# Performance work log

Hardware: AMD Instinct MI355X
Metric: run time of the kernel (lower is better)

The kernel has to match this reference:

```python
import jax, jax.numpy as jnp
import numpy as np
import math

BS, QL, KL = 2, 2048, 2048
H, D = 16, 64          # n_heads, cell_dim
QS = KS = VS = 1024    # query/key/value feature sizes
HD = H * D


def setup_inputs() -> dict:
    key = jax.random.key(0)
    ks = jax.random.split(key, 12)
    s_in = 1.0 / math.sqrt(QS)
    s_hd = 1.0 / math.sqrt(HD)
    return {
        "query": jax.random.normal(ks[0], (BS, QL, QS), jnp.float32),
        "key": jax.random.normal(ks[1], (BS, KL, KS), jnp.float32),
        "value": jax.random.normal(ks[2], (BS, KL, VS), jnp.float32),
        # nn.Linear weights stored as [in, out] for x @ W + b
        "Wq_w": jax.random.normal(ks[3], (QS, HD), jnp.float32) * s_in,
        "Wq_b": jax.random.normal(ks[4], (HD,), jnp.float32) * s_in,
        "Wk_w": jax.random.normal(ks[5], (KS, HD), jnp.float32) * s_in,
        "Wk_b": jax.random.normal(ks[6], (HD,), jnp.float32) * s_in,
        "Wv_w": jax.random.normal(ks[7], (VS, HD), jnp.float32) * s_in,
        "Wv_b": jax.random.normal(ks[8], (HD,), jnp.float32) * s_in,
        "Wo_w": jax.random.normal(ks[9], (HD, HD), jnp.float32) * s_hd,
        "Wo_b": jax.random.normal(ks[10], (HD,), jnp.float32) * s_hd,
    }


def reference(query, key, value, Wq_w, Wq_b, Wk_w, Wk_b, Wv_w, Wv_b, Wo_w, Wo_b):
    bs, ql, _ = query.shape
    kl = key.shape[1]
    # project and split heads; torch .chunk along dim 2 == head-major reshape
    q = (query @ Wq_w + Wq_b).reshape(bs, ql, H, D).transpose(0, 2, 1, 3)  # bhqd
    k = (key @ Wk_w + Wk_b).reshape(bs, kl, H, D).transpose(0, 2, 1, 3)    # bhkd
    v = (value @ Wv_w + Wv_b).reshape(bs, kl, H, D).transpose(0, 2, 1, 3)  # bhkd
    scores = jnp.einsum("bhqd,bhkd->bhqk", q, k) / jnp.sqrt(jnp.float32(D))
    # log_softmax(...).exp() == softmax (use_mask=False path)
    w = jax.nn.softmax(scores, axis=-1)
    heads = jnp.einsum("bhqk,bhkd->bhqd", w, v)
    out = heads.transpose(0, 2, 1, 3).reshape(bs, ql, HD)  # concat heads on dim 2
    return out @ Wo_w + Wo_b
```

## Files before the change

### kernel.cpp

```cpp
#include <hip/hip_runtime.h>

#define BSZ 2
#define SEQ 2048
#define NH 16
#define DHD 64
#define HDIM 1024
#define FS 1024
#define MR (BSZ*SEQ)
#define L2E 1.4426950408889634f

typedef __bf16 bf16x8 __attribute__((ext_vector_type(8)));
typedef __bf16 bf16x2t __attribute__((ext_vector_type(2)));
typedef float f32x4 __attribute__((ext_vector_type(4)));
typedef float f32x16 __attribute__((ext_vector_type(16)));
typedef unsigned short u16;
typedef unsigned int u32;
typedef u32 u32x4 __attribute__((ext_vector_type(4)));

__device__ __forceinline__ u16 f2bf(float f) {
  u32 x = __float_as_uint(f);
  return (u16)((x + 0x7fffu + ((x >> 16) & 1u)) >> 16);
}

__device__ __forceinline__ u32 pack2bf(float a, float b) {
  bf16x2t t = {(__bf16)a, (__bf16)b};
  return __builtin_bit_cast(u32, t);
}

__device__ __forceinline__ void gload16(const void* g, void* l) {
  __builtin_amdgcn_global_load_lds(
      (const __attribute__((address_space(1))) u32*)g,
      (__attribute__((address_space(3))) u32*)l, 16, 0, 0);
}

__global__ __launch_bounds__(256) void cast3_k(const float* __restrict__ q,
                                               const float* __restrict__ k,
                                               const float* __restrict__ v,
                                               u16* __restrict__ dst, int n4) {
  int i = blockIdx.x * 256 + threadIdx.x;
  const int st = gridDim.x * 256;
  const int tot = 3 * n4;
  for (; i < tot; i += st) {
    const int arr = i >> 20;
    const int idx = i & (n4 - 1);
    const float* src = arr == 0 ? q : arr == 1 ? k : v;
    float4 vv = ((const float4*)src)[idx];
    ushort4 o;
    o.x = f2bf(vv.x); o.y = f2bf(vv.y); o.z = f2bf(vv.z); o.w = f2bf(vv.w);
    ((ushort4*)dst)[i] = o;
  }
}

__global__ __launch_bounds__(256) void transw4_k(
    const float* __restrict__ W0, const float* __restrict__ W1,
    const float* __restrict__ W2, const float* __restrict__ W3,
    u16* __restrict__ WTbase) {
  __shared__ float t[32][33];
  const int z = blockIdx.z;
  const float* W = z == 0 ? W0 : z == 1 ? W1 : z == 2 ? W2 : W3;
  u16* WT = WTbase + (size_t)z * FS * HDIM;
  const int tx = threadIdx.x, ty = threadIdx.y;
  const int c0 = blockIdx.x * 32, r0 = blockIdx.y * 32;
#pragma unroll
  for (int i = 0; i < 4; i++)
    t[ty + 8 * i][tx] = W[(size_t)(r0 + ty + 8 * i) * FS + c0 + tx];
  __syncthreads();
#pragma unroll
  for (int i = 0; i < 4; i++)
    WT[(size_t)(c0 + ty + 8 * i) * FS + r0 + tx] = f2bf(t[tx][ty + 8 * i]);
}

__global__ __launch_bounds__(256, 2) void gemmQKV_k(
    const u16* __restrict__ Abase, const u16* __restrict__ WTbase,
    const float* __restrict__ bq, const float* __restrict__ bk,
    const float* __restrict__ bv, u16* __restrict__ QKbase,
    u16* __restrict__ VpT) {
  __shared__ u16 aL[128 * 64];
  __shared__ u16 bL[128 * 64];
  const int grp = blockIdx.y;
  const u16* A = Abase + (size_t)grp * MR * FS;
  const u16* BT = WTbase + (size_t)grp * FS * HDIM;
  const float* bias = grp == 0 ? bq : grp == 1 ? bk : bv;
  const int m0 = (blockIdx.x >> 3) << 7;
  const int n0 = (blockIdx.x & 7) << 7;
  const int tid = threadIdx.x, w = tid >> 6, lane = tid & 63;
  const int wr = ((w >> 1) << 6), wc = ((w & 1) << 6);
  const int li = lane & 15, g = lane >> 4;

  f32x4 acc[4][4];
#pragma unroll
  for (int i = 0; i < 4; i++)
#pragma unroll
    for (int j = 0; j < 4; j++) acc[i][j] = (f32x4){0.f, 0.f, 0.f, 0.f};

  for (int k0 = 0; k0 < FS; k0 += 64) {
#pragma unroll
    for (int j = 0; j < 4; j++) {
      const int c = w * 4 + j;
      const int r = c * 8 + (lane >> 3);
      const int sc = (lane & 7) ^ (r & 7);
      gload16(A + (size_t)(m0 + r) * FS + k0 + sc * 8, (char*)aL + c * 1024);
      gload16(BT + (size_t)(n0 + r) * FS + k0 + sc * 8, (char*)bL + c * 1024);
    }
    __syncthreads();
    bf16x8 af[2][4], bfr[2][4];
#pragma unroll
    for (int ks = 0; ks < 2; ks++) {
#pragma unroll
      for (int mf = 0; mf < 4; mf++) {
        const int r = wr + mf * 16 + li;
        const int sl = (g + 4 * ks) ^ (r & 7);
        af[ks][mf] = *(const bf16x8*)((const char*)aL + r * 128 + sl * 16);
      }
#pragma unroll
      for (int nf = 0; nf < 4; nf++) {
        const int r = wc + nf * 16 + li;
        const int sl = (g + 4 * ks) ^ (r & 7);
        bfr[ks][nf] = *(const bf16x8*)((const char*)bL + r * 128 + sl * 16);
      }
    }
#pragma unroll
    for (int ks = 0; ks < 2; ks++)
#pragma unroll
      for (int mf = 0; mf < 4; mf++)
#pragma unroll
        for (int nf = 0; nf < 4; nf++)
          acc[mf][nf] = __builtin_amdgcn_mfma_f32_16x16x32_bf16(
              af[ks][mf], bfr[ks][nf], acc[mf][nf], 0, 0, 0);
    __syncthreads();
  }

  if (grp < 2) {
    const float osc = grp == 0 ? 0.125f * L2E : 1.0f;
    u16* C = QKbase + (size_t)grp * MR * HDIM;
#pragma unroll
    for (int mf = 0; mf < 4; mf++)
#pragma unroll
      for (int nf = 0; nf < 4; nf++) {
        const int n = n0 + wc + nf * 16 + li;
        const float bvl = bias[n];
#pragma unroll
        for (int r4 = 0; r4 < 4; r4++) {
          const int m = m0 + wr + mf * 16 + g * 4 + r4;
          C[(size_t)m * HDIM + n] = f2bf((acc[mf][nf][r4] + bvl) * osc);
        }
      }
  } else {
#pragma unroll
    for (int mf = 0; mf < 4; mf++)
#pragma unroll
      for (int nf = 0; nf < 4; nf++) {
        const int n = n0 + wc + nf * 16 + li;
        const float bvl = bias[n];
        const int m = m0 + wr + mf * 16 + g * 4;
        const int bb = m >> 11, kv = m & 2047;
        ushort4 o;
        o.x = f2bf(acc[mf][nf][0] + bvl);
        o.y = f2bf(acc[mf][nf][1] + bvl);
        o.z = f2bf(acc[mf][nf][2] + bvl);
        o.w = f2bf(acc[mf][nf][3] + bvl);
        *(ushort4*)(VpT +
                    ((size_t)(bb * NH + (n >> 6)) * DHD + (n & 63)) * SEQ + kv) = o;
      }
  }
}

__global__ __launch_bounds__(256, 2) void gemm_out_k(
    const u16* __restrict__ A, const u16* __restrict__ BT,
    const float* __restrict__ bias, float* __restrict__ C) {
  __shared__ u16 aL[128 * 64];
  __shared__ u16 bL[128 * 64];
  const int m0 = (blockIdx.x >> 3) << 7;
  const int n0 = (blockIdx.x & 7) << 7;
  const int tid = threadIdx.x, w = tid >> 6, lane = tid & 63;
  const int wr = ((w >> 1) << 6), wc = ((w & 1) << 6);
  const int li = lane & 15, g = lane >> 4;

  f32x4 acc[4][4];
#pragma unroll
  for (int i = 0; i < 4; i++)
#pragma unroll
    for (int j = 0; j < 4; j++) acc[i][j] = (f32x4){0.f, 0.f, 0.f, 0.f};

  for (int k0 = 0; k0 < HDIM; k0 += 64) {
#pragma unroll
    for (int j = 0; j < 4; j++) {
      const int c = w * 4 + j;
      const int r = c * 8 + (lane >> 3);
      const int sc = (lane & 7) ^ (r & 7);
      gload16(A + (size_t)(m0 + r) * HDIM + k0 + sc * 8, (char*)aL + c * 1024);
      gload16(BT + (size_t)(n0 + r) * HDIM + k0 + sc * 8, (char*)bL + c * 1024);
    }
    __syncthreads();
    bf16x8 af[2][4], bfr[2][4];
#pragma unroll
    for (int ks = 0; ks < 2; ks++) {
#pragma unroll
      for (int mf = 0; mf < 4; mf++) {
        const int r = wr + mf * 16 + li;
        const int sl = (g + 4 * ks) ^ (r & 7);
        af[ks][mf] = *(const bf16x8*)((const char*)aL + r * 128 + sl * 16);
      }
#pragma unroll
      for (int nf = 0; nf < 4; nf++) {
        const int r = wc + nf * 16 + li;
        const int sl = (g + 4 * ks) ^ (r & 7);
        bfr[ks][nf] = *(const bf16x8*)((const char*)bL + r * 128 + sl * 16);
      }
    }
#pragma unroll
    for (int ks = 0; ks < 2; ks++)
#pragma unroll
      for (int mf = 0; mf < 4; mf++)
#pragma unroll
        for (int nf = 0; nf < 4; nf++)
          acc[mf][nf] = __builtin_amdgcn_mfma_f32_16x16x32_bf16(
              af[ks][mf], bfr[ks][nf], acc[mf][nf], 0, 0, 0);
    __syncthreads();
  }

#pragma unroll
  for (int mf = 0; mf < 4; mf++)
#pragma unroll
    for (int nf = 0; nf < 4; nf++) {
      const int n = n0 + wc + nf * 16 + li;
      const float bvl = bias[n];
#pragma unroll
      for (int r4 = 0; r4 < 4; r4++) {
        const int m = m0 + wr + mf * 16 + g * 4 + r4;
        C[(size_t)m * HDIM + n] = acc[mf][nf][r4] + bvl;
      }
    }
}

__global__ __launch_bounds__(256, 2) void attn_k(
    const u16* __restrict__ Qp, const u16* __restrict__ Kp,
    const u16* __restrict__ VpT, u16* __restrict__ Hd) {
  __shared__ u16 kbuf[2][64 * 64];
  __shared__ u16 vbuf[2][64 * 64];

  const int bid = blockIdx.x;
  const int swz = (bid & 7) * 64 + (bid >> 3);
  const int qb = swz & 15;
  const int h = (swz >> 4) & 15;
  const int b = swz >> 8;
  const int tid = threadIdx.x, w = tid >> 6, lane = tid & 63;
  const int q32 = lane & 31, hi = lane >> 5;
  const int q0 = qb << 7;
  const size_t qbase = (size_t)(b * SEQ + q0) * HDIM + (size_t)h * DHD;
  const size_t kbase = (size_t)(b * SEQ) * HDIM + (size_t)h * DHD;
  const size_t vtbase = (size_t)(b * NH + h) * DHD * SEQ;

  const int rr = lane >> 3;
  const int sc8 = ((lane & 7) ^ rr) * 8;
  const int fkey = (q32 & 7) << 4;

#pragma unroll
  for (int j = 0; j < 4; j++) {
    const int c = w * 4 + j;
    const int r = c * 8 + rr;
    gload16(Qp + qbase + (size_t)r * HDIM + sc8, (char*)kbuf + c * 1024);
  }
  __syncthreads();
  bf16x8 qf[4];
  {
    const char* qbp = (const char*)kbuf + (w * 32 + q32) * 128;
#pragma unroll
    for (int ds = 0; ds < 4; ds++)
      qf[ds] = *(const bf16x8*)(qbp + ((32 * ds + 16 * hi) ^ fkey));
  }
  __syncthreads();

  float mrun = -1e30f, lrun = 0.f;
  f32x16 o0, o1;
#pragma unroll
  for (int i = 0; i < 16; i++) { o0[i] = 0.f; o1[i] = 0.f; }

  auto stageKV = [&](int t, int buf) {
    const size_t kb = kbase + (size_t)(t * 64) * HDIM;
    const size_t vb = vtbase + (size_t)(t * 64);
#pragma unroll
    for (int j = 0; j < 2; j++) {
      const int c = w * 2 + j;
      const int r = c * 8 + rr;
      gload16(Kp + kb + (size_t)r * HDIM + sc8, (char*)kbuf[buf] + c * 1024);
      gload16(VpT + vb + (size_t)r * SEQ + sc8, (char*)vbuf[buf] + c * 1024);
    }
  };

  stageKV(0, 0);

  auto TILE = [&](int t, int par) {
    __syncthreads();
    if (t + 1 < SEQ / 64) stageKV(t + 1, par ^ 1);

    const char* kl = (const char*)kbuf[par];
    const char* vl = (const char*)vbuf[par];
    f32x16 s0, s1;
#pragma unroll
    for (int i = 0; i < 16; i++) { s0[i] = 0.f; s1[i] = 0.f; }
#pragma unroll
    for (int ds = 0; ds < 4; ds++) {
      const int off = (32 * ds + 16 * hi) ^ fkey;
      const bf16x8 ka = *(const bf16x8*)(kl + q32 * 128 + off);
      const bf16x8 kb2 = *(const bf16x8*)(kl + (32 + q32) * 128 + off);
      s0 = __builtin_amdgcn_mfma_f32_32x32x16_bf16(ka, qf[ds], s0, 0, 0, 0);
      s1 = __builtin_amdgcn_mfma_f32_32x32x16_bf16(kb2, qf[ds], s1, 0, 0, 0);
    }

    float mt[16];
#pragma unroll
    for (int i = 0; i < 16; i++) mt[i] = fmaxf(s0[i], s1[i]);
#pragma unroll
    for (int i = 0; i < 8; i++) mt[i] = fmaxf(mt[i], mt[i + 8]);
#pragma unroll
    for (int i = 0; i < 4; i++) mt[i] = fmaxf(mt[i], mt[i + 4]);
    float mx = fmaxf(fmaxf(mt[0], mt[1]), fmaxf(mt[2], mt[3]));
    mx = fmaxf(mx, __shfl_xor(mx, 32));
    if (!__all(mx <= mrun + 8.0f)) {
      const float mnew = fmaxf(mrun, mx);
      const float scl = __builtin_amdgcn_exp2f(mrun - mnew);
      mrun = mnew;
      lrun *= scl;
#pragma unroll
      for (int i = 0; i < 16; i++) { o0[i] *= scl; o1[i] *= scl; }
    }
    float p0[16], p1[16];
#pragma unroll
    for (int i = 0; i < 16; i++) {
      p0[i] = __builtin_amdgcn_exp2f(s0[i] - mrun);
      p1[i] = __builtin_amdgcn_exp2f(s1[i] - mrun);
    }
    float st[16];
#pragma unroll
    for (int i = 0; i < 16; i++) st[i] = p0[i] + p1[i];
#pragma unroll
    for (int i = 0; i < 8; i++) st[i] += st[i + 8];
#pragma unroll
    for (int i = 0; i < 4; i++) st[i] += st[i + 4];
    float rs = (st[0] + st[1]) + (st[2] + st[3]);
    rs += __shfl_xor(rs, 32);
    lrun += rs;

#pragma unroll
    for (int kvs = 0; kvs < 4; kvs++) {
      const float* ps = (kvs < 2) ? p0 : p1;
      const int rb = (kvs & 1) * 8;
      u32 w01 = pack2bf(ps[rb + 0], ps[rb + 1]);
      u32 w23 = pack2bf(ps[rb + 2], ps[rb + 3]);
      u32 w45 = pack2bf(ps[rb + 4], ps[rb + 5]);
      u32 w67 = pack2bf(ps[rb + 6], ps[rb + 7]);
      asm("v_permlane32_swap_b32 %0, %1" : "+v"(w01), "+v"(w45));
      asm("v_permlane32_swap_b32 %0, %1" : "+v"(w23), "+v"(w67));
      u32x4 uw = {w01, w23, w45, w67};
      const bf16x8 pf = __builtin_bit_cast(bf16x8, uw);
      const int off = (32 * kvs + 16 * hi) ^ fkey;
      const bf16x8 va = *(const bf16x8*)(vl + q32 * 128 + off);
      const bf16x8 vb2 = *(const bf16x8*)(vl + (32 + q32) * 128 + off);
      o0 = __builtin_amdgcn_mfma_f32_32x32x16_bf16(va, pf, o0, 0, 0, 0);
      o1 = __builtin_amdgcn_mfma_f32_32x32x16_bf16(vb2, pf, o1, 0, 0, 0);
    }
  };

#pragma unroll 1
  for (int tt = 0; tt < SEQ / 128; tt++) {
    TILE(2 * tt, 0);
    TILE(2 * tt + 1, 1);
  }

  const float inv = 1.f / lrun;
  const int q = q0 + w * 32 + q32;
  u16* orow = Hd + (size_t)(b * SEQ + q) * HDIM + (size_t)h * DHD;
#pragma unroll
  for (int rg = 0; rg < 4; rg++) {
    ushort4 ov;
    ov.x = f2bf(o0[4 * rg + 0] * inv);
    ov.y = f2bf(o0[4 * rg + 1] * inv);
    ov.z = f2bf(o0[4 * rg + 2] * inv);
    ov.w = f2bf(o0[4 * rg + 3] * inv);
    *(ushort4*)(orow + 8 * rg + 4 * hi) = ov;
    ushort4 ow;
    ow.x = f2bf(o1[4 * rg + 0] * inv);
    ow.y = f2bf(o1[4 * rg + 1] * inv);
    ow.z = f2bf(o1[4 * rg + 2] * inv);
    ow.w = f2bf(o1[4 * rg + 3] * inv);
    *(ushort4*)(orow + 32 + 8 * rg + 4 * hi) = ow;
  }
}

extern "C" void kernel_launch(void* const* d_in, const int* in_sizes, int n_in,
                              void* d_out, int out_size, void* d_ws, size_t ws_size,
                              hipStream_t stream) {
  (void)in_sizes; (void)n_in; (void)out_size; (void)ws_size;
  const float* q_in = (const float*)d_in[0];
  const float* k_in = (const float*)d_in[1];
  const float* v_in = (const float*)d_in[2];
  const float* Wq_w = (const float*)d_in[3];
  const float* Wq_b = (const float*)d_in[4];
  const float* Wk_w = (const float*)d_in[5];
  const float* Wk_b = (const float*)d_in[6];
  const float* Wv_w = (const float*)d_in[7];
  const float* Wv_b = (const float*)d_in[8];
  const float* Wo_w = (const float*)d_in[9];
  const float* Wo_b = (const float*)d_in[10];

  char* ws = (char*)d_ws;
  size_t off = 0;
  auto alloc = [&](size_t n) {
    char* p = ws + off;
    off += (n + 255) & ~(size_t)255;
    return p;
  };
  u16* qkv = (u16*)alloc((size_t)3 * MR * FS * 2);
  u16* wT = (u16*)alloc((size_t)4 * FS * HDIM * 2);
  u16* QK = (u16*)alloc((size_t)2 * MR * HDIM * 2);
  u16* VpT = (u16*)alloc((size_t)MR * HDIM * 2);
  u16* Hdp = (u16*)alloc((size_t)MR * HDIM * 2);

  const int n4 = MR * FS / 4;
  cast3_k<<<3072, 256, 0, stream>>>(q_in, k_in, v_in, qkv, n4);

  transw4_k<<<dim3(FS / 32, FS / 32, 4), dim3(32, 8), 0, stream>>>(
      Wq_w, Wk_w, Wv_w, Wo_w, wT);

  gemmQKV_k<<<dim3(256, 3), 256, 0, stream>>>(qkv, wT, Wq_b, Wk_b, Wv_b, QK,
                                              VpT);

  attn_k<<<BSZ * NH * (SEQ / 128), 256, 0, stream>>>(
      QK, QK + (size_t)MR * HDIM, VpT, Hdp);

  gemm_out_k<<<256, 256, 0, stream>>>(Hdp, wT + (size_t)3 * FS * HDIM, Wo_b,
                                      (float*)d_out);
}
```

Before: 131.9 us.

## Process two KV tiles per barrier and interleave QK with PV across tiles

The attention kernel's K/V shared-memory ring grows from two to four buffers, and each loop iteration now stages two tiles ahead behind a single barrier. Within an iteration, the second tile's QK MFMAs are issued before the first tile's PV MFMAs, so matrix work can overlap the softmax exp work. This halves the barrier count and raises instruction-level parallelism, but doubles LDS use to 64KB per block, which may limit occupancy at two blocks per CU. It also raises register pressure from holding two score sets at once.

```diff
diff --git a/kernel.cpp b/kernel.cpp
--- a/kernel.cpp
+++ b/kernel.cpp
@@ -236,8 +236,8 @@
 __global__ __launch_bounds__(256, 2) void attn_k(
     const u16* __restrict__ Qp, const u16* __restrict__ Kp,
     const u16* __restrict__ VpT, u16* __restrict__ Hd) {
-  __shared__ u16 kbuf[2][64 * 64];
-  __shared__ u16 vbuf[2][64 * 64];
+  __shared__ u16 kbuf[4][64 * 64];
+  __shared__ u16 vbuf[4][64 * 64];
 
   const int bid = blockIdx.x;
   const int swz = (bid & 7) * 64 + (bid >> 3);
@@ -288,15 +288,7 @@
     }
   };
 
-  stageKV(0, 0);
-
-  auto TILE = [&](int t, int par) {
-    __syncthreads();
-    if (t + 1 < SEQ / 64) stageKV(t + 1, par ^ 1);
-
-    const char* kl = (const char*)kbuf[par];
-    const char* vl = (const char*)vbuf[par];
-    f32x16 s0, s1;
+  auto QK = [&](const char* kl, f32x16& s0, f32x16& s1) {
 #pragma unroll
     for (int i = 0; i < 16; i++) { s0[i] = 0.f; s1[i] = 0.f; }
 #pragma unroll
@@ -307,7 +299,9 @@
       s0 = __builtin_amdgcn_mfma_f32_32x32x16_bf16(ka, qf[ds], s0, 0, 0, 0);
       s1 = __builtin_amdgcn_mfma_f32_32x32x16_bf16(kb2, qf[ds], s1, 0, 0, 0);
     }
-
+  };
+
+  auto SM = [&](const f32x16& s0, const f32x16& s1, float* p0, float* p1) {
     float mt[16];
 #pragma unroll
     for (int i = 0; i < 16; i++) mt[i] = fmaxf(s0[i], s1[i]);
@@ -325,7 +319,6 @@
 #pragma unroll
       for (int i = 0; i < 16; i++) { o0[i] *= scl; o1[i] *= scl; }
     }
-    float p0[16], p1[16];
 #pragma unroll
     for (int i = 0; i < 16; i++) {
       p0[i] = __builtin_amdgcn_exp2f(s0[i] - mrun);
@@ -341,7 +334,9 @@
     float rs = (st[0] + st[1]) + (st[2] + st[3]);
     rs += __shfl_xor(rs, 32);
     lrun += rs;
-
+  };
+
+  auto PV = [&](const char* vl, const float* p0, const float* p1) {
 #pragma unroll
     for (int kvs = 0; kvs < 4; kvs++) {
       const float* ps = (kvs < 2) ? p0 : p1;
@@ -362,10 +357,32 @@
     }
   };
 
+  stageKV(0, 0);
+  stageKV(1, 1);
+
 #pragma unroll 1
-  for (int tt = 0; tt < SEQ / 128; tt++) {
-    TILE(2 * tt, 0);
-    TILE(2 * tt + 1, 1);
+  for (int p = 0; p < SEQ / 128; p++) {
+    __syncthreads();
+    const int t0 = 2 * p;
+    if (p + 1 < SEQ / 128) {
+      stageKV(t0 + 2, (t0 + 2) & 3);
+      stageKV(t0 + 3, (t0 + 3) & 3);
+    }
+    const char* kl0 = (const char*)kbuf[t0 & 3];
+    const char* vl0 = (const char*)vbuf[t0 & 3];
+    const char* kl1 = (const char*)kbuf[(t0 + 1) & 3];
+    const char* vl1 = (const char*)vbuf[(t0 + 1) & 3];
+
+    f32x16 sa0, sa1;
+    QK(kl0, sa0, sa1);
+    float pa0[16], pa1[16];
+    SM(sa0, sa1, pa0, pa1);
+    f32x16 sb0, sb1;
+    QK(kl1, sb0, sb1);
+    PV(vl0, pa0, pa1);
+    float pb0[16], pb1[16];
+    SM(sb0, sb1, pb0, pb1);
+    PV(vl1, pb0, pb1);
   }
 
   const float inv = 1.f / lrun;
```

New measurement: 126.9 us. 3.8% less time.

## Split attention KV loop across two warp groups and merge softmax states

Applied to the files above, without the earlier changes.

The attention kernel now runs 512 threads per block, where two groups of four waves each take alternating 64-key tiles for the same 128 queries. A four-slot LDS ring buffer holds both groups' K/V tiles. At the end, the two online-softmax states (max, sum, output) are combined through shared memory before normalization. The aim is more waves per block to hide latency and to halve each wave's serial KV loop. The cost is a final merge step, doubled LDS use, and launch bounds that allow only one block per CU.

```diff
diff --git a/kernel.cpp b/kernel.cpp
--- a/kernel.cpp
+++ b/kernel.cpp
@@ -233,11 +233,11 @@
     }
 }
 
-__global__ __launch_bounds__(256, 2) void attn_k(
+__global__ __launch_bounds__(512, 1) void attn_k(
     const u16* __restrict__ Qp, const u16* __restrict__ Kp,
     const u16* __restrict__ VpT, u16* __restrict__ Hd) {
-  __shared__ u16 kbuf[2][64 * 64];
-  __shared__ u16 vbuf[2][64 * 64];
+  __shared__ u16 kbuf[4][64 * 64];
+  __shared__ u16 vbuf[4][64 * 64];
 
   const int bid = blockIdx.x;
   const int swz = (bid & 7) * 64 + (bid >> 3);
@@ -245,6 +245,7 @@
   const int h = (swz >> 4) & 15;
   const int b = swz >> 8;
   const int tid = threadIdx.x, w = tid >> 6, lane = tid & 63;
+  const int sel = w >> 2, g3 = w & 3;
   const int q32 = lane & 31, hi = lane >> 5;
   const int q0 = qb << 7;
   const size_t qbase = (size_t)(b * SEQ + q0) * HDIM + (size_t)h * DHD;
@@ -256,15 +257,15 @@
   const int fkey = (q32 & 7) << 4;
 
 #pragma unroll
-  for (int j = 0; j < 4; j++) {
-    const int c = w * 4 + j;
+  for (int j = 0; j < 2; j++) {
+    const int c = w * 2 + j;
     const int r = c * 8 + rr;
     gload16(Qp + qbase + (size_t)r * HDIM + sc8, (char*)kbuf + c * 1024);
   }
   __syncthreads();
   bf16x8 qf[4];
   {
-    const char* qbp = (const char*)kbuf + (w * 32 + q32) * 128;
+    const char* qbp = (const char*)kbuf + (g3 * 32 + q32) * 128;
 #pragma unroll
     for (int ds = 0; ds < 4; ds++)
       qf[ds] = *(const bf16x8*)(qbp + ((32 * ds + 16 * hi) ^ fkey));
@@ -276,26 +277,30 @@
 #pragma unroll
   for (int i = 0; i < 16; i++) { o0[i] = 0.f; o1[i] = 0.f; }
 
-  auto stageKV = [&](int t, int buf) {
+  auto stagePair = [&](int tp) {
+    const int t = tp + sel;
+    const int buf = t & 3;
     const size_t kb = kbase + (size_t)(t * 64) * HDIM;
     const size_t vb = vtbase + (size_t)(t * 64);
 #pragma unroll
     for (int j = 0; j < 2; j++) {
-      const int c = w * 2 + j;
+      const int c = g3 * 2 + j;
       const int r = c * 8 + rr;
       gload16(Kp + kb + (size_t)r * HDIM + sc8, (char*)kbuf[buf] + c * 1024);
       gload16(VpT + vb + (size_t)r * SEQ + sc8, (char*)vbuf[buf] + c * 1024);
     }
   };
 
-  stageKV(0, 0);
-
-  auto TILE = [&](int t, int par) {
+  stagePair(0);
+
+#pragma unroll 1
+  for (int p = 0; p < SEQ / 128; p++) {
     __syncthreads();
-    if (t + 1 < SEQ / 64) stageKV(t + 1, par ^ 1);
-
-    const char* kl = (const char*)kbuf[par];
-    const char* vl = (const char*)vbuf[par];
+    if (p + 1 < SEQ / 128) stagePair(2 * p + 2);
+    const int t = 2 * p + sel;
+    const char* kl = (const char*)kbuf[t & 3];
+    const char* vl = (const char*)vbuf[t & 3];
+
     f32x16 s0, s1;
 #pragma unroll
     for (int i = 0; i < 16; i++) { s0[i] = 0.f; s1[i] = 0.f; }
@@ -360,31 +365,48 @@
       o0 = __builtin_amdgcn_mfma_f32_32x32x16_bf16(va, pf, o0, 0, 0, 0);
       o1 = __builtin_amdgcn_mfma_f32_32x32x16_bf16(vb2, pf, o1, 0, 0, 0);
     }
-  };
-
-#pragma unroll 1
-  for (int tt = 0; tt < SEQ / 128; tt++) {
-    TILE(2 * tt, 0);
-    TILE(2 * tt + 1, 1);
-  }
-
-  const float inv = 1.f / lrun;
-  const int q = q0 + w * 32 + q32;
-  u16* orow = Hd + (size_t)(b * SEQ + q) * HDIM + (size_t)h * DHD;
-#pragma unroll
-  for (int rg = 0; rg < 4; rg++) {
-    ushort4 ov;
-    ov.x = f2bf(o0[4 * rg + 0] * inv);
-    ov.y = f2bf(o0[4 * rg + 1] * inv);
-    ov.z = f2bf(o0[4 * rg + 2] * inv);
-    ov.w = f2bf(o0[4 * rg + 3] * inv);
-    *(ushort4*)(orow + 8 * rg + 4 * hi) = ov;
-    ushort4 ow;
-    ow.x = f2bf(o1[4 * rg + 0] * inv);
-    ow.y = f2bf(o1[4 * rg + 1] * inv);
-    ow.z = f2bf(o1[4 * rg + 2] * inv);
-    ow.w = f2bf(o1[4 * rg + 3] * inv);
-    *(ushort4*)(orow + 32 + 8 * rg + 4 * hi) = ow;
+  }
+
+  __syncthreads();
+  char* mbase = (char*)kbuf + (g3 * 64 + lane) * 144;
+  if (sel == 1) {
+#pragma unroll
+    for (int i = 0; i < 4; i++) {
+      *(f32x4*)(mbase + i * 16) =
+          (f32x4){o0[4 * i], o0[4 * i + 1], o0[4 * i + 2], o0[4 * i + 3]};
+      *(f32x4*)(mbase + 64 + i * 16) =
+          (f32x4){o1[4 * i], o1[4 * i + 1], o1[4 * i + 2], o1[4 * i + 3]};
+    }
+    *(float*)(mbase + 128) = mrun;
+    *(float*)(mbase + 132) = lrun;
+  }
+  __syncthreads();
+  if (sel == 0) {
+    const float m2 = *(const float*)(mbase + 128);
+    const float l2 = *(const float*)(mbase + 132);
+    const float ms = fmaxf(mrun, m2);
+    const float f1 = __builtin_amdgcn_exp2f(mrun - ms);
+    const float f2 = __builtin_amdgcn_exp2f(m2 - ms);
+    const float inv = 1.f / (lrun * f1 + l2 * f2);
+    const int q = q0 + g3 * 32 + q32;
+    u16* orow = Hd + (size_t)(b * SEQ + q) * HDIM + (size_t)h * DHD;
+#pragma unroll
+    for (int rg = 0; rg < 4; rg++) {
+      const f32x4 a2 = *(const f32x4*)(mbase + rg * 16);
+      const f32x4 b2 = *(const f32x4*)(mbase + 64 + rg * 16);
+      ushort4 ov;
+      ov.x = f2bf((o0[4 * rg + 0] * f1 + a2[0] * f2) * inv);
+      ov.y = f2bf((o0[4 * rg + 1] * f1 + a2[1] * f2) * inv);
+      ov.z = f2bf((o0[4 * rg + 2] * f1 + a2[2] * f2) * inv);
+      ov.w = f2bf((o0[4 * rg + 3] * f1 + a2[3] * f2) * inv);
+      *(ushort4*)(orow + 8 * rg + 4 * hi) = ov;
+      ushort4 ow;
+      ow.x = f2bf((o1[4 * rg + 0] * f1 + b2[0] * f2) * inv);
+      ow.y = f2bf((o1[4 * rg + 1] * f1 + b2[1] * f2) * inv);
+      ow.z = f2bf((o1[4 * rg + 2] * f1 + b2[2] * f2) * inv);
+      ow.w = f2bf((o1[4 * rg + 3] * f1 + b2[3] * f2) * inv);
+      *(ushort4*)(orow + 32 + 8 * rg + 4 * hi) = ow;
+    }
   }
 }
 
@@ -426,7 +448,7 @@
   gemmQKV_k<<<dim3(256, 3), 256, 0, stream>>>(qkv, wT, Wq_b, Wk_b, Wv_b, QK,
                                               VpT);
 
-  attn_k<<<BSZ * NH * (SEQ / 128), 256, 0, stream>>>(
+  attn_k<<<BSZ * NH * (SEQ / 128), 512, 0, stream>>>(
       QK, QK + (size_t)MR * HDIM, VpT, Hdp);
 
   gemm_out_k<<<256, 256, 0, stream>>>(Hdp, wT + (size_t)3 * FS * HDIM, Wo_b,
```

New measurement: 126.6 us. -4.1%, faster.
